# Optimization experiments

Hardware: AMD Instinct MI355X
Metric: run time of the kernel (lower is better)

Reference implementation:

```python
import jax, jax.numpy as jnp
import numpy as np

N = 131072          # number of items ranked in one soft_rank call
CAPACITY = 3.0      # self.capcity in the torch module


def _pav_kl(y, w):
    """KL isotonic regression (non-increasing fit) via Pool-Adjacent-Violators.
    Pooled block value = logsumexp(y_block) - logsumexp(w_block).
    Matches torchsort / fast-soft-sort isotonic_kl. Sequential O(N)."""
    n = y.shape[0]

    def push(i, st):
        ly, lw, val, start, ptr = st
        ly = ly.at[ptr].set(y[i])
        lw = lw.at[ptr].set(w[i])
        val = val.at[ptr].set(y[i] - w[i])
        start = start.at[ptr].set(i)
        ptr = ptr + 1

        def cond(s):
            _, _, v, _, p = s
            return (p >= 2) & (v[p - 2] <= v[p - 1])

        def merge(s):
            ly, lw, v, stt, p = s
            ny = jnp.logaddexp(ly[p - 2], ly[p - 1])
            nw = jnp.logaddexp(lw[p - 2], lw[p - 1])
            return (ly.at[p - 2].set(ny), lw.at[p - 2].set(nw),
                    v.at[p - 2].set(ny - nw), stt, p - 1)

        return jax.lax.while_loop(cond, merge, (ly, lw, val, start, ptr))

    z = jnp.zeros((n,), y.dtype)
    st0 = (z, z, z, jnp.full((n,), n, jnp.int32), jnp.int32(0))
    ly, lw, val, start, ptr = jax.lax.fori_loop(0, n, push, st0)
    # invalidate stale stack slots, then map each element to its block value
    start = jnp.where(jnp.arange(n) < ptr, start, n)
    blk = jnp.searchsorted(start, jnp.arange(n), side='right') - 1
    return val[blk]


@jax.custom_vjp
def isotonic_kl(y, w):
    return _pav_kl(y, w)


def _iso_fwd(y, w):
    sol = _pav_kl(y, w)
    return sol, (y, w, sol)


def _iso_bwd(res, g):
    y, w, sol = res
    n = y.shape[0]
    # blocks = maximal runs of constant solution (exact equality by construction)
    blk = jnp.cumsum(jnp.concatenate([jnp.array([True]), sol[1:] != sol[:-1]])) - 1
    gsum = jax.ops.segment_sum(g, blk, num_segments=n)

    def seg_softmax(v):
        m = jax.ops.segment_max(v, blk, num_segments=n)
        lse = jnp.log(jax.ops.segment_sum(jnp.exp(v - m[blk]), blk, num_segments=n)) + m
        return jnp.exp(v - lse[blk])

    return seg_softmax(y) * gsum[blk], -seg_softmax(w) * gsum[blk]


isotonic_kl.defvjp(_iso_fwd, _iso_bwd)


def soft_rank_kl(scores):
    """torchsort.soft_rank(scores[None], regularization='kl'), strength=1, ascending."""
    n = scores.shape[0]
    w_log = jnp.log(jnp.arange(n, 0, -1, dtype=scores.dtype))  # log([n, ..., 1])
    perm = jnp.argsort(-scores)          # descending, stable
    s = scores[perm]
    sol = isotonic_kl(s, w_log)
    inv = jnp.argsort(perm)
    return jnp.exp(s - sol)[inv]


def setup_inputs() -> dict:
    key = jax.random.key(0)
    k = jax.random.split(key, 5)
    x = jax.random.normal(k[0], (N, 1), jnp.float32)
    # torch Linear default init bounds: 1/sqrt(fan_in)
    w1 = jax.random.uniform(k[1], (1, 32), jnp.float32, -1.0, 1.0)
    b1 = jax.random.uniform(k[2], (32,), jnp.float32, -1.0, 1.0)
    lim2 = 1.0 / np.sqrt(32.0)
    w2 = jax.random.uniform(k[3], (32, 1), jnp.float32, -lim2, lim2)
    b2 = jax.random.uniform(k[4], (1,), jnp.float32, -lim2, lim2)
    return {"x": x, "w1": w1, "b1": b1, "w2": w2, "b2": b2}


def reference(x, w1, b1, w2, b2):
    h = jnp.maximum(x @ w1 + b1, 0.0)            # [N, 32]
    scores = (h @ w2 + b2).reshape(-1)           # [N]
    ranks = soft_rank_kl(scores)                 # [N]
    other = jax.lax.stop_gradient(ranks) % CAPACITY
    ranks = (ranks - other) / CAPACITY + 1.0
    return ranks.reshape(-1, 1)
```

## Files before the change

kernel.cpp:

```cpp
#include <hip/hip_runtime.h>
#include <stdint.h>

typedef unsigned int u32;
typedef unsigned long long u64;

#define N_ITEMS 131072
#define NB 131072
#define NSLICE 4
#define MBLK 64
#define BUCK_PER_BLK 2048
#define CH_PER_BLK 32
#define PAD 65
#define REGSLOT 2048
#define FIXSCALE 268435456.0f
#define FIXMASK ((1ull << 46) - 1)


__device__ __forceinline__ float wsumf(int s, int e) {
  return 0.5f * (float)(e - s + 1) * (float)(2 * N_ITEMS - s - e);
}

__device__ __forceinline__ float key_to_score(u32 key) {
  u32 m = ~key;
  u32 u = (m & 0x80000000u) ? (m ^ 0x80000000u) : ~m;
  return __uint_as_float(u);
}

#define LOG2E 1.4426950408889634f
__device__ __forceinline__ float fexp(float x) { return exp2f(x * LOG2E); }

__device__ __forceinline__ u32 bucket_of(u32 key, u32 kmin, u32 kmax) {
  double scale = (double)NB / ((double)(kmax - kmin) + 1.0);
  u32 b = (u32)((double)(key - kmin) * scale);
  return b < NB ? b : (NB - 1);
}

__device__ __forceinline__ float recSY(int2 r) { return __int_as_float(r.y); }


__global__ __launch_bounds__(256) void score_key_kernel(
    const float* __restrict__ x,
    const float* __restrict__ w1, const float* __restrict__ b1,
    const float* __restrict__ w2, const float* __restrict__ b2,
    u32* __restrict__ keyRaw, u32* __restrict__ agg) {
  __shared__ u32 wmn[4], wmx[4];
  int t = threadIdx.x;
  int i = blockIdx.x * 256 + t;
  float xv = x[i];
  float s = b2[0];
#pragma unroll
  for (int j = 0; j < 32; ++j) {
    float h = fmaf(xv, w1[j], b1[j]);
    h = fmaxf(h, 0.0f);
    s = fmaf(h, w2[j], s);
  }
  u32 u = __float_as_uint(s);
  u32 m = u ^ ((u & 0x80000000u) ? 0xFFFFFFFFu : 0x80000000u);
  u32 key = ~m;
  keyRaw[i] = key;
  u32 mn = key, mx = key;
#pragma unroll
  for (int off = 32; off > 0; off >>= 1) {
    mn = min(mn, (u32)__shfl_xor((int)mn, off));
    mx = max(mx, (u32)__shfl_xor((int)mx, off));
  }
  if ((t & 63) == 0) { wmn[t >> 6] = mn; wmx[t >> 6] = mx; }
  __syncthreads();
  if (t == 0) {
    mn = min(min(wmn[0], wmn[1]), min(wmn[2], wmn[3]));
    mx = max(max(wmx[0], wmx[1]), max(wmx[2], wmx[3]));
    atomicMax(&agg[0], ~mn);
    atomicMax(&agg[1], mx);
  }
}


__global__ __launch_bounds__(256) void hist_kernel(
    const u32* __restrict__ keyRaw, const u32* __restrict__ agg,
    u64* __restrict__ hist8) {
  int t = threadIdx.x;
  int i = blockIdx.x * 256 + t;
  u32 kmin = ~agg[0], kmax = agg[1];
  u32 key = keyRaw[i];
  u32 g = bucket_of(key, kmin, kmax);
  float smax = key_to_score(kmin);
  float v = fexp(key_to_score(key) - smax);
  u64 fix = (u64)fmaxf(1.0f, fmaf(v, FIXSCALE, 0.5f));
  size_t slice = (size_t)(blockIdx.x & (NSLICE - 1)) * NB;
  atomicAdd(&hist8[slice + g], (1ull << 46) | fix);
}


__global__ __launch_bounds__(256) void solve_kernel(
    const u64* __restrict__ hist8, u64* __restrict__ flags, u64* __restrict__ flag2,
    u32* __restrict__ cdf, int2* __restrict__ REC,
    const u32* __restrict__ keyRaw, const u32* __restrict__ agg,
    float* __restrict__ out) {
  __shared__ u32 vals[BUCK_PER_BLK + 1];
  __shared__ float seL[BUCK_PER_BLK];
  __shared__ int   rST[CH_PER_BLK * PAD];
  __shared__ float rSY[CH_PER_BLK * PAD];
  __shared__ u32 sh[256];
  __shared__ u32 aggS[64];
  __shared__ u32 regS[65];
  __shared__ int lcnt[CH_PER_BLK];
  __shared__ int ca[16], cb[16], cM[16];
  __shared__ int shInt[4];
  int t = threadIdx.x, b = blockIdx.x;
  int B0 = b * BUCK_PER_BLK;
  for (int q = 0; q < 8; ++q) {
    int ii = q * 256 + t;
    u64 acc = 0;
#pragma unroll
    for (int c = 0; c < NSLICE; ++c) acc += hist8[(size_t)c * NB + B0 + ii];
    vals[ii] = (u32)(acc >> 46);
    seL[ii] = (float)(acc & FIXMASK) * (1.0f / FIXSCALE);
  }
  __syncthreads();
  u32 loc[8]; u32 s = 0;
  for (int q = 0; q < 8; ++q) { loc[q] = s; s += vals[t * 8 + q]; }
  sh[t] = s;
  __syncthreads();
  for (int off = 1; off < 256; off <<= 1) {
    u32 x2 = (t >= off) ? sh[t - off] : 0u;
    __syncthreads();
    sh[t] += x2;
    __syncthreads();
  }
  if (t == 0) atomicExch(&flags[b], (1ull << 32) | (u64)sh[255]);
  if (t < 64) {
    u64 f;
    do { f = atomicAdd(&flags[t], 0ull); } while ((u32)(f >> 32) == 0u);
    aggS[t] = (u32)f;
  }
  __syncthreads();
  if (t < 64) {
    u32 v = aggS[t];
    u32 inc = v;
    for (int off = 1; off < 64; off <<= 1) {
      u32 o2 = __shfl_up(inc, off);
      if (t >= off) inc += o2;
    }
    regS[t] = inc - v;
    if (t == 63) regS[64] = inc;
  }
  __syncthreads();
  u32 exclu = regS[b];
  u32 tbase = ((t == 0) ? 0u : sh[t - 1]) + exclu;
  u32 eb8[8];
  for (int q = 0; q < 8; ++q) { eb8[q] = tbase + loc[q]; vals[t * 8 + q] = eb8[q]; }
  {
    uint4* c4 = (uint4*)(cdf + B0 + t * 8);
    c4[0] = make_uint4(eb8[0], eb8[1], eb8[2], eb8[3]);
    c4[1] = make_uint4(eb8[4], eb8[5], eb8[6], eb8[7]);
  }
  if (t == 255) vals[BUCK_PER_BLK] = exclu + sh[255];
  __syncthreads();
  if (t < CH_PER_BLK) {
    int base = t * PAD;
    int ptr = 0; bool have = false;
    float syT = 0.0f; int stT = 0;
    for (int k = 0; k < 64; ++k) {
      u32 cs = vals[t * 64 + k], ce = vals[t * 64 + k + 1];
      if (ce == cs) continue;
      float syC = seL[t * 64 + k];
      int stC = (int)cs, eC = (int)ce - 1;
      while (have) {
        float SWc = wsumf(stC, eC);
        float SWt = wsumf(stT, stC - 1);
        if (!(syT * SWc <= syC * SWt)) break;
        syC += syT; stC = stT;
        if (ptr == 0) { have = false; break; }
        --ptr;
        stT = rST[base + ptr]; syT = rSY[base + ptr];
      }
      if (have) { rST[base + ptr] = stT; rSY[base + ptr] = syT; ++ptr; }
      stT = stC; syT = syC; have = true;
    }
    if (have) { rST[base + ptr] = stT; rSY[base + ptr] = syT; ++ptr; }
    lcnt[t] = ptr;
  }
  __syncthreads();
  for (int j = 0; j < 5; ++j) {
    int P = CH_PER_BLK >> (j + 1);
    if (t < P) {
      int p = t;
      int kL = p << (j + 1), kR = kL + (1 << j);
      int slotL = kL * PAD, slotR = kR * PAD;
      int nL = lcnt[kL], nR = lcnt[kR];
      int a = 0, bb = 0, hasM = 0;
      if (nL > 0 && nR > 0) {
        int gstartR = (int)vals[kR * 64];
        int gendR   = (int)vals[(kR + (1 << j)) * 64];
        float SYL = rSY[slotL + nL - 1]; int stL = rST[slotL + nL - 1];
        float SYR = rSY[slotR];
        int eR = (nR > 1) ? (rST[slotR + 1] - 1) : (gendR - 1);
        float SWL = wsumf(stL, gstartR - 1);
        float SWR = wsumf(gstartR, eR);
        if (SYL * SWR <= SYR * SWL) {
          hasM = 1;
          float SYM = SYL + SYR; int Ms = stL, Me = eR;
          a = 1; bb = 1;
          for (;;) {
            float SWM = wsumf(Ms, Me);
            if (a < nL) {
              float SYe = rSY[slotL + nL - 1 - a]; int ste = rST[slotL + nL - 1 - a];
              float SWe = wsumf(ste, Ms - 1);
              if (SYe * SWM <= SYM * SWe) { SYM += SYe; Ms = ste; ++a; continue; }
            }
            if (bb < nR) {
              float SYb = rSY[slotR + bb]; int sb = rST[slotR + bb];
              int eb = (bb + 1 < nR) ? (rST[slotR + bb + 1] - 1) : (gendR - 1);
              float SWb = wsumf(sb, eb);
              if (SYM * SWb <= SYb * SWM) { SYM += SYb; Me = eb; ++bb; continue; }
            }
            break;
          }
          rST[slotL + nL - a] = Ms; rSY[slotL + nL - a] = SYM;
        }
      }
      ca[p] = a; cb[p] = bb; cM[p] = hasM;
    }
    __syncthreads();
    {
      int w = t >> 6, lane = t & 63;
      for (int p = w; p < P; p += 4) {
        int kL = p << (j + 1), kR = kL + (1 << j);
        int nL = lcnt[kL], nR = lcnt[kR];
        int a = ca[p], bb = cb[p], hasM = cM[p];
        int destBase = kL * PAD + nL - a + hasM;
        int srcBase = kR * PAD + bb;
        int ncopy = nR - bb;
        for (int off = 0; off < ncopy; off += 64) {
          int k2 = off + lane; bool act = k2 < ncopy;
          int vt = 0; float vs = 0.f;
          if (act) { vt = rST[srcBase + k2]; vs = rSY[srcBase + k2]; }
          if (act) { rST[destBase + k2] = vt; rSY[destBase + k2] = vs; }
        }
      }
    }
    __syncthreads();
    if (t < P) {
      int p = t; int kL = p << (j + 1), kR = kL + (1 << j);
      lcnt[kL] = lcnt[kL] - ca[p] + cM[p] + (lcnt[kR] - cb[p]);
    }
    __syncthreads();
  }
  int myCnt = lcnt[0];
  for (int k = t; k < myCnt; k += 256)
    REC[(size_t)b * REGSLOT + k] = make_int2(rST[k], __float_as_int(rSY[k]));
  __syncthreads();
  int lvl = 0;
  for (;;) {
    if (b & (1 << lvl)) {
      __threadfence();
      if (t == 0) atomicExch(&flag2[b], (1ull << 32) | (u64)(u32)myCnt);
      break;
    }
    if (lvl == 6) {
      __threadfence();
      if (t == 0) atomicExch(&flag2[0], (2ull << 32) | (u64)(u32)myCnt);
      break;
    }
    int pb = b + (1 << lvl);
    if (t == 0) {
      u64 f;
      do { f = atomicAdd(&flag2[pb], 0ull); __builtin_amdgcn_s_sleep(1); } while ((f >> 32) == 0ull);
      shInt[0] = (int)(u32)f;
    }
    __syncthreads();
    __threadfence();
    int nR = shInt[0];
    int nL = myCnt;
    int slotL = b * REGSLOT, slotR = pb * REGSLOT;
    if (t == 0) {
      int a = 0, bb = 0, hasM = 0;
      if (nL > 0 && nR > 0) {
        int gstartR = (int)regS[pb];
        int gendR   = (int)regS[b + (2 << lvl)];
        int2 rL = REC[slotL + nL - 1];
        float SYL = recSY(rL); int stL = rL.x;
        int2 rR = REC[slotR];
        float SYR = recSY(rR);
        int eR = (nR > 1) ? (REC[slotR + 1].x - 1) : (gendR - 1);
        float SWL = wsumf(stL, gstartR - 1);
        float SWR = wsumf(gstartR, eR);
        if (SYL * SWR <= SYR * SWL) {
          hasM = 1;
          float SYM = SYL + SYR; int Ms = stL, Me = eR;
          a = 1; bb = 1;
          for (;;) {
            float SWM = wsumf(Ms, Me);
            if (a < nL) {
              int2 re = REC[slotL + nL - 1 - a];
              float SYe = recSY(re); int ste = re.x;
              float SWe = wsumf(ste, Ms - 1);
              if (SYe * SWM <= SYM * SWe) { SYM += SYe; Ms = ste; ++a; continue; }
            }
            if (bb < nR) {
              int2 rb = REC[slotR + bb];
              float SYb = recSY(rb); int sb = rb.x;
              int eb = (bb + 1 < nR) ? (REC[slotR + bb + 1].x - 1) : (gendR - 1);
              float SWb = wsumf(sb, eb);
              if (SYM * SWb <= SYb * SWM) { SYM += SYb; Me = eb; ++bb; continue; }
            }
            break;
          }
          REC[slotL + nL - a] = make_int2(Ms, __float_as_int(SYM));
        }
      }
      shInt[1] = a; shInt[2] = bb; shInt[3] = hasM;
    }
    __syncthreads();
    int a = shInt[1], bb = shInt[2], hasM = shInt[3];
    int destBase = slotL + nL - a + hasM;
    int srcBase = slotR + bb;
    int ncopy = nR - bb;
    for (int off = 0; off < ncopy; off += 256) {
      int k2 = off + t; bool act = k2 < ncopy;
      int2 vr = make_int2(0, 0);
      if (act) vr = REC[srcBase + k2];
      __syncthreads();
      if (act) REC[destBase + k2] = vr;
      __syncthreads();
    }
    __syncthreads();
    myCnt = nL - a + hasM + (nR - bb);
    ++lvl;
  }
  if (t == 0) {
    u64 f;
    do { f = atomicAdd(&flag2[0], 0ull); __builtin_amdgcn_s_sleep(2); } while ((f >> 32) != 2ull);
    shInt[0] = (int)(u32)f;
  }
  __syncthreads();
  __threadfence();
  int m = shInt[0];
  bool useL = (m <= CH_PER_BLK * PAD);
  if (useL) {
    for (int k = t; k < m; k += 256) {
      int2 r = REC[k];
      rST[k] = r.x; rSY[k] = __int_as_float(r.y);
    }
  }
  __syncthreads();
  u32 kmin = ~agg[0], kmax = agg[1];
  float smax = key_to_score(kmin);
  for (int q = 0; q < 8; ++q) {
    int i = b * 2048 + q * 256 + t;
    u32 key = keyRaw[i];
    u32 g = bucket_of(key, kmin, kmax);
    int p = (int)cdf[g];
    int lo = 0, hi = m - 1;
    if (useL) {
      while (lo < hi) {
        int mid = (lo + hi + 1) >> 1;
        if (rST[mid] <= p) lo = mid; else hi = mid - 1;
      }
      int s0 = rST[lo];
      int e0 = (lo + 1 < m) ? (rST[lo + 1] - 1) : (N_ITEMS - 1);
      float SW = wsumf(s0, e0);
      float sc = key_to_score(key);
      float rank = fexp(sc - smax) * SW / rSY[lo];
      out[i] = floorf(rank * (1.0f / 3.0f)) + 1.0f;
    } else {
      while (lo < hi) {
        int mid = (lo + hi + 1) >> 1;
        if (REC[mid].x <= p) lo = mid; else hi = mid - 1;
      }
      int2 r = REC[lo];
      int s0 = r.x;
      int e0 = (lo + 1 < m) ? (REC[lo + 1].x - 1) : (N_ITEMS - 1);
      float SW = wsumf(s0, e0);
      float sc = key_to_score(key);
      float rank = fexp(sc - smax) * SW / recSY(r);
      out[i] = floorf(rank * (1.0f / 3.0f)) + 1.0f;
    }
  }
}


extern "C" void kernel_launch(void* const* d_in, const int* in_sizes, int n_in,
                              void* d_out, int out_size, void* d_ws, size_t ws_size,
                              hipStream_t stream) {
  const float* x  = (const float*)d_in[0];
  const float* w1 = (const float*)d_in[1];
  const float* b1 = (const float*)d_in[2];
  const float* w2 = (const float*)d_in[3];
  const float* b2 = (const float*)d_in[4];
  float* out = (float*)d_out;

  char* ws = (char*)d_ws;
  size_t o = 0;
  u32* cdf    = (u32*)(ws + o); o += (size_t)(NB + 4) * 4;
  u32* keyRaw = (u32*)(ws + o); o += (size_t)N_ITEMS * 4;
  int2* REC   = (int2*)(ws + o); o += (size_t)N_ITEMS * 8;
  char* zbase = ws + o;
  u64* hist8  = (u64*)(ws + o); o += (size_t)NSLICE * NB * 8;
  u64* flags  = (u64*)(ws + o); o += (size_t)MBLK * 8;
  u64* flag2  = (u64*)(ws + o); o += (size_t)MBLK * 8;
  u32* agg    = (u32*)(ws + o); o += 64;
  size_t zbytes = (size_t)((ws + o) - zbase);

  hipMemsetAsync(zbase, 0, zbytes, stream);
  score_key_kernel<<<512, 256, 0, stream>>>(x, w1, b1, w2, b2, keyRaw, agg);
  hist_kernel<<<512, 256, 0, stream>>>(keyRaw, agg, hist8);
  solve_kernel<<<MBLK, 256, 0, stream>>>(hist8, flags, flag2, cdf, REC, keyRaw, agg, out);
}
```

Measured before the change: 142.9 us.

## Fuse score and histogram kernels with grid barrier, widen solve to 512 blocks

Merges the score and histogram kernels into one launch that uses a spin-wait grid barrier and clears the single histogram in-kernel instead of through a memset. Drops the four histogram slices in favour of one shared histogram. The solve kernel now launches 512 blocks: 64 do the scan and PAV work, and the rest wait on per-block cdf-ready flags and each write one output element. The old 6-level cross-block merge tree becomes a two-level 8-way merge, and the block-wide scan uses wave shuffles. Flags are padded to separate cache lines and read with relaxed agent-scope atomic loads. This removes a launch and memset traffic and spreads the output phase across more CUs, at the cost of relying on all 512 blocks being co-resident for the barriers and of more atomic contention on the single histogram.

```diff
diff --git a/kernel.cpp b/kernel.cpp
--- a/kernel.cpp
+++ b/kernel.cpp
@@ -6,12 +6,13 @@
 
 #define N_ITEMS 131072
 #define NB 131072
-#define NSLICE 4
 #define MBLK 64
+#define NBLK 512
 #define BUCK_PER_BLK 2048
 #define CH_PER_BLK 32
 #define PAD 65
 #define REGSLOT 2048
+#define FPAD 16
 #define FIXSCALE 268435456.0f
 #define FIXMASK ((1ull << 46) - 1)
 
@@ -37,15 +38,21 @@
 
 __device__ __forceinline__ float recSY(int2 r) { return __int_as_float(r.y); }
 
-
-__global__ __launch_bounds__(256) void score_key_kernel(
+__device__ __forceinline__ u64 agent_ld(const u64* p) {
+  return __hip_atomic_load(p, __ATOMIC_RELAXED, __HIP_MEMORY_SCOPE_AGENT);
+}
+
+
+__global__ __launch_bounds__(256) void score_hist_kernel(
     const float* __restrict__ x,
     const float* __restrict__ w1, const float* __restrict__ b1,
     const float* __restrict__ w2, const float* __restrict__ b2,
-    u32* __restrict__ keyRaw, u32* __restrict__ agg) {
+    u32* __restrict__ keyRaw, u32* __restrict__ agg, u64* __restrict__ hist,
+    u64* __restrict__ bar, u64* __restrict__ rel) {
   __shared__ u32 wmn[4], wmx[4];
   int t = threadIdx.x;
   int i = blockIdx.x * 256 + t;
+  ((uint2*)hist)[i] = make_uint2(0u, 0u);
   float xv = x[i];
   float s = b2[0];
 #pragma unroll
@@ -55,8 +62,8 @@
     s = fmaf(h, w2[j], s);
   }
   u32 u = __float_as_uint(s);
-  u32 m = u ^ ((u & 0x80000000u) ? 0xFFFFFFFFu : 0x80000000u);
-  u32 key = ~m;
+  u32 mb = u ^ ((u & 0x80000000u) ? 0xFFFFFFFFu : 0x80000000u);
+  u32 key = ~mb;
   keyRaw[i] = key;
   u32 mn = key, mx = key;
 #pragma unroll
@@ -71,28 +78,35 @@
     mx = max(max(wmx[0], wmx[1]), max(wmx[2], wmx[3]));
     atomicMax(&agg[0], ~mn);
     atomicMax(&agg[1], mx);
-  }
-}
-
-
-__global__ __launch_bounds__(256) void hist_kernel(
-    const u32* __restrict__ keyRaw, const u32* __restrict__ agg,
-    u64* __restrict__ hist8) {
-  int t = threadIdx.x;
-  int i = blockIdx.x * 256 + t;
+    __threadfence();
+    atomicExch(&bar[(size_t)blockIdx.x * FPAD], 1ull);
+  }
+  if (blockIdx.x == 0) {
+    u64 f;
+    do { f = agent_ld(&bar[(size_t)t * FPAD]); } while (f == 0ull);
+    do { f = agent_ld(&bar[(size_t)(t + 256) * FPAD]); } while (f == 0ull);
+    __syncthreads();
+    if (t == 0) { __threadfence(); atomicExch(rel, 1ull); }
+  } else {
+    if (t == 0) {
+      u64 f;
+      do { f = agent_ld(rel); __builtin_amdgcn_s_sleep(1); } while (f == 0ull);
+    }
+    __syncthreads();
+  }
+  __threadfence();
   u32 kmin = ~agg[0], kmax = agg[1];
-  u32 key = keyRaw[i];
   u32 g = bucket_of(key, kmin, kmax);
   float smax = key_to_score(kmin);
   float v = fexp(key_to_score(key) - smax);
   u64 fix = (u64)fmaxf(1.0f, fmaf(v, FIXSCALE, 0.5f));
-  size_t slice = (size_t)(blockIdx.x & (NSLICE - 1)) * NB;
-  atomicAdd(&hist8[slice + g], (1ull << 46) | fix);
+  atomicAdd(&hist[g], (1ull << 46) | fix);
 }
 
 
 __global__ __launch_bounds__(256) void solve_kernel(
-    const u64* __restrict__ hist8, u64* __restrict__ flags, u64* __restrict__ flag2,
+    const u64* __restrict__ hist, u64* __restrict__ flags, u64* __restrict__ cdfrdy,
+    u64* __restrict__ flag2, u64* __restrict__ grpf,
     u32* __restrict__ cdf, int2* __restrict__ REC,
     const u32* __restrict__ keyRaw, const u32* __restrict__ agg,
     float* __restrict__ out) {
@@ -100,242 +114,317 @@
   __shared__ float seL[BUCK_PER_BLK];
   __shared__ int   rST[CH_PER_BLK * PAD];
   __shared__ float rSY[CH_PER_BLK * PAD];
-  __shared__ u32 sh[256];
-  __shared__ u32 aggS[64];
+  __shared__ u32 wsum[4];
   __shared__ u32 regS[65];
   __shared__ int lcnt[CH_PER_BLK];
   __shared__ int ca[16], cb[16], cM[16];
-  __shared__ int shInt[4];
+  __shared__ int shInt[12];
   int t = threadIdx.x, b = blockIdx.x;
-  int B0 = b * BUCK_PER_BLK;
-  for (int q = 0; q < 8; ++q) {
-    int ii = q * 256 + t;
-    u64 acc = 0;
+  u32 kmin = ~agg[0], kmax = agg[1];
+  float smax = key_to_score(kmin);
+  int oi = b * 256 + t;
+  u32 okey = keyRaw[oi];
+  u32 og = bucket_of(okey, kmin, kmax);
+  float oexp = fexp(key_to_score(okey) - smax);
+  int p_ = 0;
+
+  if (b >= MBLK) {
+    {
+      u64 f;
+      do {
+        f = agent_ld(&cdfrdy[(size_t)(t & 63) * FPAD]);
+        if (f == 0ull) __builtin_amdgcn_s_sleep(32);
+      } while (f == 0ull);
+    }
+    __syncthreads();
+    __threadfence();
+    p_ = (int)cdf[og];
+  } else {
+    int B0 = b * BUCK_PER_BLK;
+    for (int q = 0; q < 8; ++q) {
+      int ii = q * 256 + t;
+      u64 acc = hist[(size_t)B0 + ii];
+      vals[ii] = (u32)(acc >> 46);
+      seL[ii] = (float)(acc & FIXMASK) * (1.0f / FIXSCALE);
+    }
+    __syncthreads();
+    u32 loc[8]; u32 s = 0;
+    for (int q = 0; q < 8; ++q) { loc[q] = s; s += vals[t * 8 + q]; }
+    u32 inc = s;
 #pragma unroll
-    for (int c = 0; c < NSLICE; ++c) acc += hist8[(size_t)c * NB + B0 + ii];
-    vals[ii] = (u32)(acc >> 46);
-    seL[ii] = (float)(acc & FIXMASK) * (1.0f / FIXSCALE);
-  }
-  __syncthreads();
-  u32 loc[8]; u32 s = 0;
-  for (int q = 0; q < 8; ++q) { loc[q] = s; s += vals[t * 8 + q]; }
-  sh[t] = s;
-  __syncthreads();
-  for (int off = 1; off < 256; off <<= 1) {
-    u32 x2 = (t >= off) ? sh[t - off] : 0u;
-    __syncthreads();
-    sh[t] += x2;
-    __syncthreads();
-  }
-  if (t == 0) atomicExch(&flags[b], (1ull << 32) | (u64)sh[255]);
-  if (t < 64) {
-    u64 f;
-    do { f = atomicAdd(&flags[t], 0ull); } while ((u32)(f >> 32) == 0u);
-    aggS[t] = (u32)f;
-  }
-  __syncthreads();
-  if (t < 64) {
-    u32 v = aggS[t];
-    u32 inc = v;
     for (int off = 1; off < 64; off <<= 1) {
-      u32 o2 = __shfl_up(inc, off);
-      if (t >= off) inc += o2;
-    }
-    regS[t] = inc - v;
-    if (t == 63) regS[64] = inc;
-  }
-  __syncthreads();
-  u32 exclu = regS[b];
-  u32 tbase = ((t == 0) ? 0u : sh[t - 1]) + exclu;
-  u32 eb8[8];
-  for (int q = 0; q < 8; ++q) { eb8[q] = tbase + loc[q]; vals[t * 8 + q] = eb8[q]; }
-  {
-    uint4* c4 = (uint4*)(cdf + B0 + t * 8);
-    c4[0] = make_uint4(eb8[0], eb8[1], eb8[2], eb8[3]);
-    c4[1] = make_uint4(eb8[4], eb8[5], eb8[6], eb8[7]);
-  }
-  if (t == 255) vals[BUCK_PER_BLK] = exclu + sh[255];
-  __syncthreads();
-  if (t < CH_PER_BLK) {
-    int base = t * PAD;
-    int ptr = 0; bool have = false;
-    float syT = 0.0f; int stT = 0;
-    for (int k = 0; k < 64; ++k) {
-      u32 cs = vals[t * 64 + k], ce = vals[t * 64 + k + 1];
-      if (ce == cs) continue;
-      float syC = seL[t * 64 + k];
-      int stC = (int)cs, eC = (int)ce - 1;
-      while (have) {
-        float SWc = wsumf(stC, eC);
-        float SWt = wsumf(stT, stC - 1);
-        if (!(syT * SWc <= syC * SWt)) break;
-        syC += syT; stC = stT;
-        if (ptr == 0) { have = false; break; }
-        --ptr;
-        stT = rST[base + ptr]; syT = rSY[base + ptr];
+      u32 o2 = (u32)__shfl_up((int)inc, off);
+      if ((t & 63) >= off) inc += o2;
+    }
+    if ((t & 63) == 63) wsum[t >> 6] = inc;
+    __syncthreads();
+    u32 w = (u32)(t >> 6);
+    u32 woff = 0;
+    if (w > 0) woff += wsum[0];
+    if (w > 1) woff += wsum[1];
+    if (w > 2) woff += wsum[2];
+    u32 total = wsum[0] + wsum[1] + wsum[2] + wsum[3];
+    u32 texcl = woff + inc - s;
+    if (t == 0) atomicExch(&flags[(size_t)b * FPAD], (1ull << 32) | (u64)total);
+    if (t < 64) {
+      u64 f;
+      do { f = agent_ld(&flags[(size_t)t * FPAD]); } while ((u32)(f >> 32) == 0u);
+      u32 v = (u32)f, inc2 = v;
+#pragma unroll
+      for (int off = 1; off < 64; off <<= 1) {
+        u32 o2 = (u32)__shfl_up((int)inc2, off);
+        if (t >= off) inc2 += o2;
+      }
+      regS[t] = inc2 - v;
+      if (t == 63) regS[64] = inc2;
+    }
+    __syncthreads();
+    u32 exclu = regS[b];
+    u32 tbase = texcl + exclu;
+    u32 eb8[8];
+    for (int q = 0; q < 8; ++q) { eb8[q] = tbase + loc[q]; vals[t * 8 + q] = eb8[q]; }
+    {
+      uint4* c4 = (uint4*)(cdf + B0 + t * 8);
+      c4[0] = make_uint4(eb8[0], eb8[1], eb8[2], eb8[3]);
+      c4[1] = make_uint4(eb8[4], eb8[5], eb8[6], eb8[7]);
+    }
+    if (t == 255) vals[BUCK_PER_BLK] = exclu + total;
+    __syncthreads();
+    if (t == 0) { __threadfence(); atomicExch(&cdfrdy[(size_t)b * FPAD], 1ull); }
+    if (t < CH_PER_BLK) {
+      int base = t * PAD;
+      int ptr = 0; bool have = false;
+      float syT = 0.0f; int stT = 0;
+      for (int k = 0; k < 64; ++k) {
+        u32 cs = vals[t * 64 + k], ce = vals[t * 64 + k + 1];
+        if (ce == cs) continue;
+        float syC = seL[t * 64 + k];
+        int stC = (int)cs, eC = (int)ce - 1;
+        while (have) {
+          float SWc = wsumf(stC, eC);
+          float SWt = wsumf(stT, stC - 1);
+          if (!(syT * SWc <= syC * SWt)) break;
+          syC += syT; stC = stT;
+          if (ptr == 0) { have = false; break; }
+          --ptr;
+          stT = rST[base + ptr]; syT = rSY[base + ptr];
+        }
+        if (have) { rST[base + ptr] = stT; rSY[base + ptr] = syT; ++ptr; }
+        stT = stC; syT = syC; have = true;
       }
       if (have) { rST[base + ptr] = stT; rSY[base + ptr] = syT; ++ptr; }
-      stT = stC; syT = syC; have = true;
-    }
-    if (have) { rST[base + ptr] = stT; rSY[base + ptr] = syT; ++ptr; }
-    lcnt[t] = ptr;
-  }
-  __syncthreads();
-  for (int j = 0; j < 5; ++j) {
-    int P = CH_PER_BLK >> (j + 1);
-    if (t < P) {
-      int p = t;
-      int kL = p << (j + 1), kR = kL + (1 << j);
-      int slotL = kL * PAD, slotR = kR * PAD;
-      int nL = lcnt[kL], nR = lcnt[kR];
-      int a = 0, bb = 0, hasM = 0;
-      if (nL > 0 && nR > 0) {
-        int gstartR = (int)vals[kR * 64];
-        int gendR   = (int)vals[(kR + (1 << j)) * 64];
-        float SYL = rSY[slotL + nL - 1]; int stL = rST[slotL + nL - 1];
-        float SYR = rSY[slotR];
-        int eR = (nR > 1) ? (rST[slotR + 1] - 1) : (gendR - 1);
-        float SWL = wsumf(stL, gstartR - 1);
-        float SWR = wsumf(gstartR, eR);
-        if (SYL * SWR <= SYR * SWL) {
-          hasM = 1;
-          float SYM = SYL + SYR; int Ms = stL, Me = eR;
-          a = 1; bb = 1;
-          for (;;) {
-            float SWM = wsumf(Ms, Me);
-            if (a < nL) {
-              float SYe = rSY[slotL + nL - 1 - a]; int ste = rST[slotL + nL - 1 - a];
-              float SWe = wsumf(ste, Ms - 1);
-              if (SYe * SWM <= SYM * SWe) { SYM += SYe; Ms = ste; ++a; continue; }
+      lcnt[t] = ptr;
+    }
+    __syncthreads();
+    for (int j = 0; j < 5; ++j) {
+      int P = CH_PER_BLK >> (j + 1);
+      if (t < P) {
+        int p = t;
+        int kL = p << (j + 1), kR = kL + (1 << j);
+        int slotL = kL * PAD, slotR = kR * PAD;
+        int nL = lcnt[kL], nR = lcnt[kR];
+        int a = 0, bb = 0, hasM = 0;
+        if (nL > 0 && nR > 0) {
+          int gstartR = (int)vals[kR * 64];
+          int gendR   = (int)vals[(kR + (1 << j)) * 64];
+          float SYL = rSY[slotL + nL - 1]; int stL = rST[slotL + nL - 1];
+          float SYR = rSY[slotR];
+          int eR = (nR > 1) ? (rST[slotR + 1] - 1) : (gendR - 1);
+          float SWL = wsumf(stL, gstartR - 1);
+          float SWR = wsumf(gstartR, eR);
+          if (SYL * SWR <= SYR * SWL) {
+            hasM = 1;
+            float SYM = SYL + SYR; int Ms = stL, Me = eR;
+            a = 1; bb = 1;
+            for (;;) {
+              float SWM = wsumf(Ms, Me);
+              if (a < nL) {
+                float SYe = rSY[slotL + nL - 1 - a]; int ste = rST[slotL + nL - 1 - a];
+                float SWe = wsumf(ste, Ms - 1);
+                if (SYe * SWM <= SYM * SWe) { SYM += SYe; Ms = ste; ++a; continue; }
+              }
+              if (bb < nR) {
+                float SYb = rSY[slotR + bb]; int sb = rST[slotR + bb];
+                int eb = (bb + 1 < nR) ? (rST[slotR + bb + 1] - 1) : (gendR - 1);
+                float SWb = wsumf(sb, eb);
+                if (SYM * SWb <= SYb * SWM) { SYM += SYb; Me = eb; ++bb; continue; }
+              }
+              break;
             }
-            if (bb < nR) {
-              float SYb = rSY[slotR + bb]; int sb = rST[slotR + bb];
-              int eb = (bb + 1 < nR) ? (rST[slotR + bb + 1] - 1) : (gendR - 1);
-              float SWb = wsumf(sb, eb);
-              if (SYM * SWb <= SYb * SWM) { SYM += SYb; Me = eb; ++bb; continue; }
+            rST[slotL + nL - a] = Ms; rSY[slotL + nL - a] = SYM;
+          }
+        }
+        ca[p] = a; cb[p] = bb; cM[p] = hasM;
+      }
+      __syncthreads();
+      {
+        int wv = t >> 6, lane = t & 63;
+        for (int p = wv; p < P; p += 4) {
+          int kL = p << (j + 1), kR = kL + (1 << j);
+          int nL = lcnt[kL], nR = lcnt[kR];
+          int a = ca[p], bb = cb[p], hasM = cM[p];
+          int destBase = kL * PAD + nL - a + hasM;
+          int srcBase = kR * PAD + bb;
+          int ncopy = nR - bb;
+          for (int off = 0; off < ncopy; off += 64) {
+            int k2 = off + lane; bool act = k2 < ncopy;
+            int vt = 0; float vs = 0.f;
+            if (act) { vt = rST[srcBase + k2]; vs = rSY[srcBase + k2]; }
+            if (act) { rST[destBase + k2] = vt; rSY[destBase + k2] = vs; }
+          }
+        }
+      }
+      __syncthreads();
+      if (t < P) {
+        int p = t; int kL = p << (j + 1), kR = kL + (1 << j);
+        lcnt[kL] = lcnt[kL] - ca[p] + cM[p] + (lcnt[kR] - cb[p]);
+      }
+      __syncthreads();
+    }
+    int myCnt = lcnt[0];
+    for (int k = t; k < myCnt; k += 256)
+      REC[(size_t)b * REGSLOT + k] = make_int2(rST[k], __float_as_int(rSY[k]));
+    __syncthreads();
+    if (t == 0) { __threadfence(); atomicExch(&flag2[(size_t)b * FPAD], (1ull << 32) | (u64)(u32)myCnt); }
+    if ((b & 7) == 0) {
+      if (t < 7) {
+        u64 f;
+        do { f = agent_ld(&flag2[(size_t)(b + 1 + t) * FPAD]); } while ((u32)(f >> 32) == 0u);
+        shInt[4 + t] = (int)(u32)f;
+      }
+      __syncthreads();
+      __threadfence();
+      int nL = myCnt;
+      int slotL = b * REGSLOT;
+      for (int k = 1; k < 8; ++k) {
+        int nR = shInt[4 + k - 1];
+        int slotR = (b + k) * REGSLOT;
+        int gstartR = (int)regS[b + k];
+        int gendR   = (int)regS[b + k + 1];
+        if (t == 0) {
+          int a = 0, bb = 0, hasM = 0;
+          if (nL > 0 && nR > 0) {
+            int2 rL = REC[slotL + nL - 1];
+            float SYL = recSY(rL); int stL = rL.x;
+            int2 rR = REC[slotR];
+            float SYR = recSY(rR);
+            int eR = (nR > 1) ? (REC[slotR + 1].x - 1) : (gendR - 1);
+            float SWL = wsumf(stL, gstartR - 1);
+            float SWR = wsumf(gstartR, eR);
+            if (SYL * SWR <= SYR * SWL) {
+              hasM = 1;
+              float SYM = SYL + SYR; int Ms = stL, Me = eR;
+              a = 1; bb = 1;
+              for (;;) {
+                float SWM = wsumf(Ms, Me);
+                if (a < nL) {
+                  int2 re = REC[slotL + nL - 1 - a];
+                  float SYe = recSY(re); int ste = re.x;
+                  float SWe = wsumf(ste, Ms - 1);
+                  if (SYe * SWM <= SYM * SWe) { SYM += SYe; Ms = ste; ++a; continue; }
+                }
+                if (bb < nR) {
+                  int2 rb = REC[slotR + bb];
+                  float SYb = recSY(rb); int sb = rb.x;
+                  int eb = (bb + 1 < nR) ? (REC[slotR + bb + 1].x - 1) : (gendR - 1);
+                  float SWb = wsumf(sb, eb);
+                  if (SYM * SWb <= SYb * SWM) { SYM += SYb; Me = eb; ++bb; continue; }
+                }
+                break;
+              }
+              REC[slotL + nL - a] = make_int2(Ms, __float_as_int(SYM));
             }
-            break;
           }
-          rST[slotL + nL - a] = Ms; rSY[slotL + nL - a] = SYM;
+          shInt[0] = a; shInt[1] = bb; shInt[2] = hasM;
         }
-      }
-      ca[p] = a; cb[p] = bb; cM[p] = hasM;
-    }
-    __syncthreads();
-    {
-      int w = t >> 6, lane = t & 63;
-      for (int p = w; p < P; p += 4) {
-        int kL = p << (j + 1), kR = kL + (1 << j);
-        int nL = lcnt[kL], nR = lcnt[kR];
-        int a = ca[p], bb = cb[p], hasM = cM[p];
-        int destBase = kL * PAD + nL - a + hasM;
-        int srcBase = kR * PAD + bb;
+        __syncthreads();
+        int a = shInt[0], bb = shInt[1], hasM = shInt[2];
+        int destBase = slotL + nL - a + hasM;
+        int srcBase = slotR + bb;
         int ncopy = nR - bb;
-        for (int off = 0; off < ncopy; off += 64) {
-          int k2 = off + lane; bool act = k2 < ncopy;
-          int vt = 0; float vs = 0.f;
-          if (act) { vt = rST[srcBase + k2]; vs = rSY[srcBase + k2]; }
-          if (act) { rST[destBase + k2] = vt; rSY[destBase + k2] = vs; }
+        for (int k2 = t; k2 < ncopy; k2 += 256) REC[destBase + k2] = REC[srcBase + k2];
+        nL = nL - a + hasM + ncopy;
+        __syncthreads();
+      }
+      myCnt = nL;
+      if (t == 0) { __threadfence(); atomicExch(&grpf[(size_t)(b >> 3) * FPAD], (1ull << 32) | (u64)(u32)myCnt); }
+    }
+    if (b == 0) {
+      if (t < 7) {
+        u64 f;
+        do { f = agent_ld(&grpf[(size_t)(1 + t) * FPAD]); } while ((u32)(f >> 32) == 0u);
+        shInt[4 + t] = (int)(u32)f;
+      }
+      __syncthreads();
+      __threadfence();
+      int nL = myCnt;
+      int slotL = 0;
+      for (int k = 1; k < 8; ++k) {
+        int nR = shInt[4 + k - 1];
+        int slotR = (k * 8) * REGSLOT;
+        int gstartR = (int)regS[k * 8];
+        int gendR   = (int)regS[k * 8 + 8];
+        if (t == 0) {
+          int a = 0, bb = 0, hasM = 0;
+          if (nL > 0 && nR > 0) {
+            int2 rL = REC[slotL + nL - 1];
+            float SYL = recSY(rL); int stL = rL.x;
+            int2 rR = REC[slotR];
+            float SYR = recSY(rR);
+            int eR = (nR > 1) ? (REC[slotR + 1].x - 1) : (gendR - 1);
+            float SWL = wsumf(stL, gstartR - 1);
+            float SWR = wsumf(gstartR, eR);
+            if (SYL * SWR <= SYR * SWL) {
+              hasM = 1;
+              float SYM = SYL + SYR; int Ms = stL, Me = eR;
+              a = 1; bb = 1;
+              for (;;) {
+                float SWM = wsumf(Ms, Me);
+                if (a < nL) {
+                  int2 re = REC[slotL + nL - 1 - a];
+                  float SYe = recSY(re); int ste = re.x;
+                  float SWe = wsumf(ste, Ms - 1);
+                  if (SYe * SWM <= SYM * SWe) { SYM += SYe; Ms = ste; ++a; continue; }
+                }
+                if (bb < nR) {
+                  int2 rb = REC[slotR + bb];
+                  float SYb = recSY(rb); int sb = rb.x;
+                  int eb = (bb + 1 < nR) ? (REC[slotR + bb + 1].x - 1) : (gendR - 1);
+                  float SWb = wsumf(sb, eb);
+                  if (SYM * SWb <= SYb * SWM) { SYM += SYb; Me = eb; ++bb; continue; }
+                }
+                break;
+              }
+              REC[slotL + nL - a] = make_int2(Ms, __float_as_int(SYM));
+            }
+          }
+          shInt[0] = a; shInt[1] = bb; shInt[2] = hasM;
         }
-      }
-    }
-    __syncthreads();
-    if (t < P) {
-      int p = t; int kL = p << (j + 1), kR = kL + (1 << j);
-      lcnt[kL] = lcnt[kL] - ca[p] + cM[p] + (lcnt[kR] - cb[p]);
-    }
-    __syncthreads();
-  }
-  int myCnt = lcnt[0];
-  for (int k = t; k < myCnt; k += 256)
-    REC[(size_t)b * REGSLOT + k] = make_int2(rST[k], __float_as_int(rSY[k]));
-  __syncthreads();
-  int lvl = 0;
-  for (;;) {
-    if (b & (1 << lvl)) {
-      __threadfence();
-      if (t == 0) atomicExch(&flag2[b], (1ull << 32) | (u64)(u32)myCnt);
-      break;
-    }
-    if (lvl == 6) {
-      __threadfence();
-      if (t == 0) atomicExch(&flag2[0], (2ull << 32) | (u64)(u32)myCnt);
-      break;
-    }
-    int pb = b + (1 << lvl);
-    if (t == 0) {
-      u64 f;
-      do { f = atomicAdd(&flag2[pb], 0ull); __builtin_amdgcn_s_sleep(1); } while ((f >> 32) == 0ull);
-      shInt[0] = (int)(u32)f;
-    }
-    __syncthreads();
-    __threadfence();
-    int nR = shInt[0];
-    int nL = myCnt;
-    int slotL = b * REGSLOT, slotR = pb * REGSLOT;
-    if (t == 0) {
-      int a = 0, bb = 0, hasM = 0;
-      if (nL > 0 && nR > 0) {
-        int gstartR = (int)regS[pb];
-        int gendR   = (int)regS[b + (2 << lvl)];
-        int2 rL = REC[slotL + nL - 1];
-        float SYL = recSY(rL); int stL = rL.x;
-        int2 rR = REC[slotR];
-        float SYR = recSY(rR);
-        int eR = (nR > 1) ? (REC[slotR + 1].x - 1) : (gendR - 1);
-        float SWL = wsumf(stL, gstartR - 1);
-        float SWR = wsumf(gstartR, eR);
-        if (SYL * SWR <= SYR * SWL) {
-          hasM = 1;
-          float SYM = SYL + SYR; int Ms = stL, Me = eR;
-          a = 1; bb = 1;
-          for (;;) {
-            float SWM = wsumf(Ms, Me);
-            if (a < nL) {
-              int2 re = REC[slotL + nL - 1 - a];
-              float SYe = recSY(re); int ste = re.x;
-              float SWe = wsumf(ste, Ms - 1);
-              if (SYe * SWM <= SYM * SWe) { SYM += SYe; Ms = ste; ++a; continue; }
-            }
-            if (bb < nR) {
-              int2 rb = REC[slotR + bb];
-              float SYb = recSY(rb); int sb = rb.x;
-              int eb = (bb + 1 < nR) ? (REC[slotR + bb + 1].x - 1) : (gendR - 1);
-              float SWb = wsumf(sb, eb);
-              if (SYM * SWb <= SYb * SWM) { SYM += SYb; Me = eb; ++bb; continue; }
-            }
-            break;
-          }
-          REC[slotL + nL - a] = make_int2(Ms, __float_as_int(SYM));
-        }
-      }
-      shInt[1] = a; shInt[2] = bb; shInt[3] = hasM;
-    }
-    __syncthreads();
-    int a = shInt[1], bb = shInt[2], hasM = shInt[3];
-    int destBase = slotL + nL - a + hasM;
-    int srcBase = slotR + bb;
-    int ncopy = nR - bb;
-    for (int off = 0; off < ncopy; off += 256) {
-      int k2 = off + t; bool act = k2 < ncopy;
-      int2 vr = make_int2(0, 0);
-      if (act) vr = REC[srcBase + k2];
-      __syncthreads();
-      if (act) REC[destBase + k2] = vr;
-      __syncthreads();
-    }
-    __syncthreads();
-    myCnt = nL - a + hasM + (nR - bb);
-    ++lvl;
-  }
+        __syncthreads();
+        int a = shInt[0], bb = shInt[1], hasM = shInt[2];
+        int destBase = slotL + nL - a + hasM;
+        int srcBase = slotR + bb;
+        int ncopy = nR - bb;
+        for (int k2 = t; k2 < ncopy; k2 += 256) REC[destBase + k2] = REC[srcBase + k2];
+        nL = nL - a + hasM + ncopy;
+        __syncthreads();
+      }
+      if (t == 0) { __threadfence(); atomicExch(&grpf[(size_t)8 * FPAD], (2ull << 32) | (u64)(u32)nL); }
+    }
+  }
+
   if (t == 0) {
     u64 f;
-    do { f = atomicAdd(&flag2[0], 0ull); __builtin_amdgcn_s_sleep(2); } while ((f >> 32) != 2ull);
+    do {
+      f = agent_ld(&grpf[(size_t)8 * FPAD]);
+      if ((f >> 32) != 2ull) __builtin_amdgcn_s_sleep(2);
+    } while ((f >> 32) != 2ull);
     shInt[0] = (int)(u32)f;
   }
   __syncthreads();
   __threadfence();
   int m = shInt[0];
+  if (b < MBLK) p_ = (int)cdf[og];
   bool useL = (m <= CH_PER_BLK * PAD);
   if (useL) {
     for (int k = t; k < m; k += 256) {
@@ -344,38 +433,28 @@
     }
   }
   __syncthreads();
-  u32 kmin = ~agg[0], kmax = agg[1];
-  float smax = key_to_score(kmin);
-  for (int q = 0; q < 8; ++q) {
-    int i = b * 2048 + q * 256 + t;
-    u32 key = keyRaw[i];
-    u32 g = bucket_of(key, kmin, kmax);
-    int p = (int)cdf[g];
-    int lo = 0, hi = m - 1;
-    if (useL) {
-      while (lo < hi) {
-        int mid = (lo + hi + 1) >> 1;
-        if (rST[mid] <= p) lo = mid; else hi = mid - 1;
-      }
-      int s0 = rST[lo];
-      int e0 = (lo + 1 < m) ? (rST[lo + 1] - 1) : (N_ITEMS - 1);
-      float SW = wsumf(s0, e0);
-      float sc = key_to_score(key);
-      float rank = fexp(sc - smax) * SW / rSY[lo];
-      out[i] = floorf(rank * (1.0f / 3.0f)) + 1.0f;
-    } else {
-      while (lo < hi) {
-        int mid = (lo + hi + 1) >> 1;
-        if (REC[mid].x <= p) lo = mid; else hi = mid - 1;
-      }
-      int2 r = REC[lo];
-      int s0 = r.x;
-      int e0 = (lo + 1 < m) ? (REC[lo + 1].x - 1) : (N_ITEMS - 1);
-      float SW = wsumf(s0, e0);
-      float sc = key_to_score(key);
-      float rank = fexp(sc - smax) * SW / recSY(r);
-      out[i] = floorf(rank * (1.0f / 3.0f)) + 1.0f;
-    }
+  int lo = 0, hi = m - 1;
+  if (useL) {
+    while (lo < hi) {
+      int mid = (lo + hi + 1) >> 1;
+      if (rST[mid] <= p_) lo = mid; else hi = mid - 1;
+    }
+    int s0 = rST[lo];
+    int e0 = (lo + 1 < m) ? (rST[lo + 1] - 1) : (N_ITEMS - 1);
+    float SW = wsumf(s0, e0);
+    float rank = oexp * SW / rSY[lo];
+    out[oi] = floorf(rank * (1.0f / 3.0f)) + 1.0f;
+  } else {
+    while (lo < hi) {
+      int mid = (lo + hi + 1) >> 1;
+      if (REC[mid].x <= p_) lo = mid; else hi = mid - 1;
+    }
+    int2 r = REC[lo];
+    int s0 = r.x;
+    int e0 = (lo + 1 < m) ? (REC[lo + 1].x - 1) : (N_ITEMS - 1);
+    float SW = wsumf(s0, e0);
+    float rank = oexp * SW / recSY(r);
+    out[oi] = floorf(rank * (1.0f / 3.0f)) + 1.0f;
   }
 }
 
@@ -395,15 +474,19 @@
   u32* cdf    = (u32*)(ws + o); o += (size_t)(NB + 4) * 4;
   u32* keyRaw = (u32*)(ws + o); o += (size_t)N_ITEMS * 4;
   int2* REC   = (int2*)(ws + o); o += (size_t)N_ITEMS * 8;
+  u64* hist   = (u64*)(ws + o); o += (size_t)NB * 8;
   char* zbase = ws + o;
-  u64* hist8  = (u64*)(ws + o); o += (size_t)NSLICE * NB * 8;
-  u64* flags  = (u64*)(ws + o); o += (size_t)MBLK * 8;
-  u64* flag2  = (u64*)(ws + o); o += (size_t)MBLK * 8;
+  u64* bar    = (u64*)(ws + o); o += (size_t)NBLK * FPAD * 8;
+  u64* rel    = (u64*)(ws + o); o += (size_t)FPAD * 8;
+  u64* flags  = (u64*)(ws + o); o += (size_t)MBLK * FPAD * 8;
+  u64* cdfrdy = (u64*)(ws + o); o += (size_t)MBLK * FPAD * 8;
+  u64* flag2  = (u64*)(ws + o); o += (size_t)MBLK * FPAD * 8;
+  u64* grpf   = (u64*)(ws + o); o += (size_t)9 * FPAD * 8;
   u32* agg    = (u32*)(ws + o); o += 64;
   size_t zbytes = (size_t)((ws + o) - zbase);
 
   hipMemsetAsync(zbase, 0, zbytes, stream);
-  score_key_kernel<<<512, 256, 0, stream>>>(x, w1, b1, w2, b2, keyRaw, agg);
-  hist_kernel<<<512, 256, 0, stream>>>(keyRaw, agg, hist8);
-  solve_kernel<<<MBLK, 256, 0, stream>>>(hist8, flags, flag2, cdf, REC, keyRaw, agg, out);
-}
+  score_hist_kernel<<<NBLK, 256, 0, stream>>>(x, w1, b1, w2, b2, keyRaw, agg, hist, bar, rel);
+  solve_kernel<<<NBLK, 256, 0, stream>>>(hist, flags, cdfrdy, flag2, grpf,
+                                         cdf, REC, keyRaw, agg, out);
+}
```

Result: slower. 207.8 us (+45.5%).
